# Optimization experiments

Measured on AMD Instinct MI355X. Metric: run time of the kernel, lower is better.

## Reference

```python
import jax, jax.numpy as jnp
import numpy as np

Q_HEADS, KV_HEADS, DIMS, IN_DIMS = 16, 4, 1024, 1024
HEAD_D = DIMS // Q_HEADS            # 64
GROUPS = Q_HEADS // KV_HEADS        # 4
ROPE_BASE = 10000.0


def nd_rope(x, coords):
    """N-D rotary embedding.
    x: [..., s, d]; coords: broadcastable [..., s, a] (float).
    Head dim d is split into a contiguous chunks of d//a; within each chunk
    consecutive pairs (2i, 2i+1) are rotated by angle coord_axis * base^(-2i/(d//a)).
    """
    a = coords.shape[-1]
    d = x.shape[-1]
    dpa = d // a                                  # dims per coordinate axis (even)
    inv_freq = ROPE_BASE ** (-jnp.arange(dpa // 2, dtype=jnp.float32) * (2.0 / dpa))
    angles = coords[..., :, None] * inv_freq      # [..., s, a, dpa//2]
    angles = angles.reshape(angles.shape[:-2] + (d // 2,))
    cos, sin = jnp.cos(angles), jnp.sin(angles)
    xp = x.reshape(x.shape[:-1] + (d // 2, 2))
    x1, x2 = xp[..., 0], xp[..., 1]
    return jnp.stack([x1 * cos - x2 * sin, x1 * sin + x2 * cos], axis=-1).reshape(x.shape)


def setup_inputs() -> dict:
    key = jax.random.key(0)
    k1, k2, k3, k4, k5, k6, k7, k8 = jax.random.split(key, 8)
    B, SQ, SKV, A = 4, 2048, 2048, 2
    q = jax.random.normal(k1, (B, SQ, IN_DIMS), dtype=jnp.float32)
    kv = jax.random.normal(k2, (B, SKV, IN_DIMS), dtype=jnp.float32)
    q_coords = jax.random.randint(k3, (B, SQ, A), 0, 2048, dtype=jnp.int32)
    kv_coords = jax.random.randint(k4, (B, SKV, A), 0, 2048, dtype=jnp.int32)
    s_in = 1.0 / np.sqrt(IN_DIMS)
    Wq = jax.random.normal(k5, (IN_DIMS, Q_HEADS, HEAD_D), dtype=jnp.float32) * s_in
    Wk = jax.random.normal(k6, (IN_DIMS, KV_HEADS, HEAD_D), dtype=jnp.float32) * s_in
    Wv = jax.random.normal(k7, (IN_DIMS, KV_HEADS, HEAD_D), dtype=jnp.float32) * s_in
    Wo = jax.random.normal(k8, (KV_HEADS * HEAD_D, IN_DIMS), dtype=jnp.float32) * (1.0 / np.sqrt(KV_HEADS * HEAD_D))
    return {"q": q, "q_coords": q_coords, "kv": kv, "kv_coords": kv_coords,
            "Wq": Wq, "Wk": Wk, "Wv": Wv, "Wo": Wo}


def reference(q, q_coords, kv, kv_coords, Wq, Wk, Wv, Wo):
    B, SQ = q.shape[0], q.shape[1]
    qp = jnp.einsum('bsi,ihd->bshd', q, Wq)   # [b, sq, q_heads, hd]
    kp = jnp.einsum('bsi,ihd->bshd', kv, Wk)  # [b, skv, kv_heads, hd]
    vp = jnp.einsum('bsi,ihd->bshd', kv, Wv)
    # '... s (h g) d -> ... g h s d' with h=KV_HEADS outer, g=GROUPS inner
    qp = qp.reshape(B, SQ, KV_HEADS, GROUPS, HEAD_D).transpose(0, 3, 2, 1, 4)  # [b,g,h,sq,hd]
    kp = kp.transpose(0, 2, 1, 3)  # [b,h,skv,hd]
    vp = vp.transpose(0, 2, 1, 3)
    qc = q_coords.astype(jnp.float32)[:, None, None]  # [b,1,1,sq,a] -> broadcast over g,h
    kc = kv_coords.astype(jnp.float32)[:, None]       # [b,1,skv,a] -> broadcast over h
    qr = nd_rope(qp, qc)
    kr = nd_rope(kp, kc)
    # NOTE: einops pattern omits g in output -> group axis is SUMMED (faithful to source)
    scores = jnp.einsum('bghsd,bhad->bhsa', qr, kr) / (HEAD_D ** 0.5)
    attn = jax.nn.softmax(scores, axis=-1)
    out = jnp.einsum('bhsa,bhad->bhsd', attn, vp)
    out = out.transpose(0, 2, 1, 3).reshape(B, SQ, KV_HEADS * HEAD_D)
    return out @ Wo
```

## Files before the change

### kernel.cpp

```cpp
#include <hip/hip_runtime.h>

#define BATCH 4
#define SEQQ  2048
#define SEQKV 2048
#define NH    4
#define HD    64
#define IND   1024
#define QSCL 0.18033688011112042f

typedef __attribute__((ext_vector_type(8))) short short8;
typedef __attribute__((ext_vector_type(4))) short s4v;
typedef __attribute__((ext_vector_type(4))) float floatx4;

#if defined(__HIP_DEVICE_COMPILE__) && __has_builtin(__builtin_amdgcn_exp2f)
  #define EXP2(x) __builtin_amdgcn_exp2f(x)
#else
  #define EXP2(x) exp2f(x)
#endif

#if defined(__HIP_DEVICE_COMPILE__)
  #if __has_builtin(__builtin_amdgcn_mfma_f32_16x16x16bf16_1k)
    #define MFMA16(a, b, c) __builtin_amdgcn_mfma_f32_16x16x16bf16_1k(a, b, c, 0, 0, 0)
  #elif __has_builtin(__builtin_amdgcn_mfma_f32_16x16x16_bf16)
    #define MFMA16(a, b, c) __builtin_amdgcn_mfma_f32_16x16x16_bf16(a, b, c, 0, 0, 0)
  #else
    #error "no 16x16x16 bf16 MFMA builtin on gfx950 device pass"
  #endif
#else
  #define MFMA16(a, b, c) (c)
#endif
#define MFMA32(a, b, c) __builtin_amdgcn_mfma_f32_16x16x32_bf16(a, b, c, 0, 0, 0)

__device__ __forceinline__ short f2b(float f) {
    unsigned u; __builtin_memcpy(&u, &f, 4);
    u = (u + 0x7fffu + ((u >> 16) & 1u)) >> 16;
    return (short)u;
}
__device__ __forceinline__ short8 cvt8(const float* p) {
    float4 a = *(const float4*)p;
    float4 b = *(const float4*)(p + 4);
    short8 r;
    r[0] = f2b(a.x); r[1] = f2b(a.y); r[2] = f2b(a.z); r[3] = f2b(a.w);
    r[4] = f2b(b.x); r[5] = f2b(b.y); r[6] = f2b(b.z); r[7] = f2b(b.w);
    return r;
}

__global__ __launch_bounds__(256) void prep_all(
    const float* __restrict__ Wq, const float* __restrict__ Wk,
    const float* __restrict__ Wv, const float* __restrict__ Wo,
    const float* __restrict__ q, const float* __restrict__ kv,
    short* __restrict__ Wq_t, short* __restrict__ Wkv_t, short* __restrict__ Wo_t,
    short* __restrict__ qb, short* __restrict__ kvb) {
    __shared__ short Ts[64][65];
    int blk = blockIdx.x;
    if (blk < 256) {
        int c4 = threadIdx.x & 63, r4 = threadIdx.x >> 6;
        if (blk < 64) {
            int h = blk & 3, ib = blk >> 2;
#pragma unroll 4
            for (int jj = 0; jj < 16; ++jj) {
                int il = r4 * 16 + jj;
                float s = 0.f;
#pragma unroll
                for (int g = 0; g < 4; ++g)
                    s += Wq[(ib * 64 + il) * 1024 + (h * 4 + g) * 64 + c4];
                Ts[il][c4] = f2b(s);
            }
            __syncthreads();
#pragma unroll 4
            for (int jj = 0; jj < 16; ++jj) {
                int dl = r4 * 16 + jj;
                Wq_t[(h * 64 + dl) * 1024 + ib * 64 + c4] = Ts[c4][dl];
            }
        } else if (blk < 192) {
            int t = blk - 64, ss = t >> 6; t &= 63;
            int ib = t >> 2, nb = t & 3;
            const float* W = ss ? Wv : Wk;
#pragma unroll 4
            for (int jj = 0; jj < 16; ++jj) {
                int il = r4 * 16 + jj;
                Ts[il][c4] = f2b(W[(ib * 64 + il) * 256 + nb * 64 + c4]);
            }
            __syncthreads();
#pragma unroll 4
            for (int jj = 0; jj < 16; ++jj) {
                int dl = r4 * 16 + jj;
                Wkv_t[(ss * 256 + nb * 64 + dl) * 1024 + ib * 64 + c4] = Ts[c4][dl];
            }
        } else {
            int t = blk - 192, kb = t >> 4, nb = t & 15;
#pragma unroll 4
            for (int jj = 0; jj < 16; ++jj) {
                int il = r4 * 16 + jj;
                Ts[il][c4] = f2b(Wo[(kb * 64 + il) * 1024 + nb * 64 + c4]);
            }
            __syncthreads();
#pragma unroll 4
            for (int jj = 0; jj < 16; ++jj) {
                int dl = r4 * 16 + jj;
                Wo_t[(nb * 64 + dl) * 256 + kb * 64 + c4] = Ts[c4][dl];
            }
        }
    } else if (blk < 2304) {
        long e = ((long)(blk - 256) * 256 + threadIdx.x) * 16;
        *(short8*)(qb + e)     = cvt8(q + e);
        *(short8*)(qb + e + 8) = cvt8(q + e + 8);
    } else {
        long e = ((long)(blk - 2304) * 256 + threadIdx.x) * 16;
        *(short8*)(kvb + e)     = cvt8(kv + e);
        *(short8*)(kvb + e + 8) = cvt8(kv + e + 8);
    }
}

template <int MODE>
__device__ __forceinline__ void gemm64(
    const short* __restrict__ A, const short* __restrict__ Wt,
    int m0, int n0, short* As, short* Bs,
    const int* __restrict__ coords, short* __restrict__ ropeDst,
    short* __restrict__ vDst) {
    const int t = threadIdx.x;
    const int w = t >> 6, lane = t & 63, ln = lane & 15, quad = lane >> 4;
    const int srow8 = lane >> 3;
    const int schk = (lane & 7) ^ (srow8 & 7);
    const int ln7 = ln & 7;
    floatx4 acc[2][4];
#pragma unroll
    for (int mt = 0; mt < 2; ++mt)
#pragma unroll
        for (int nt = 0; nt < 4; ++nt) acc[mt][nt] = floatx4{0.f, 0.f, 0.f, 0.f};

    auto stage = [&](int ks, int sel) {
#pragma unroll
        for (int i = 0; i < 4; ++i)
            __builtin_amdgcn_global_load_lds(
                (const void*)(A + (long)(m0 + w * 32 + i * 8 + srow8) * 1024 + ks + schk * 8),
                (void*)(As + sel * 8192 + (w * 32 + i * 8) * 64), 16, 0, 0);
#pragma unroll
        for (int i = 0; i < 2; ++i)
            __builtin_amdgcn_global_load_lds(
                (const void*)(Wt + (long)(n0 + w * 16 + i * 8 + srow8) * 1024 + ks + schk * 8),
                (void*)(Bs + sel * 4096 + (w * 16 + i * 8) * 64), 16, 0, 0);
    };

    stage(0, 0);
    __syncthreads();
    int cur = 0;
    for (int tt = 0; tt < 16; ++tt) {
        if (tt < 15) stage((tt + 1) * 64, cur ^ 1);
        const short* Ac = As + cur * 8192;
        const short* Bc = Bs + cur * 4096;
        short8 af[2][2], bf[4][2];
#pragma unroll
        for (int mt = 0; mt < 2; ++mt)
#pragma unroll
            for (int kc = 0; kc < 2; ++kc)
                af[mt][kc] = *(const short8*)(Ac + (w * 32 + mt * 16 + ln) * 64
                                              + ((kc * 4 + quad) ^ ln7) * 8);
#pragma unroll
        for (int nt = 0; nt < 4; ++nt)
#pragma unroll
            for (int kc = 0; kc < 2; ++kc)
                bf[nt][kc] = *(const short8*)(Bc + (nt * 16 + ln) * 64
                                              + ((kc * 4 + quad) ^ ln7) * 8);
#pragma unroll
        for (int kc = 0; kc < 2; ++kc)
#pragma unroll
            for (int mt = 0; mt < 2; ++mt)
#pragma unroll
                for (int nt = 0; nt < 4; ++nt)
                    acc[mt][nt] = MFMA32(af[mt][kc], bf[nt][kc], acc[mt][nt]);
        __syncthreads();
        cur ^= 1;
    }

    if (MODE == 1 || n0 < 256) {
        const int h = (n0 >> 6) & 3;
        const float scl = (MODE == 1) ? QSCL : 1.0f;
        const float L = -0.5756462732485114f;
        const float fA = __expf((float)(ln >> 1) * L);
        const float fB = __expf((float)(8 + (ln >> 1)) * L);
        const float sgn = (ln & 1) ? 1.0f : -1.0f;
#pragma unroll
        for (int mt = 0; mt < 2; ++mt) {
            int row0 = m0 + w * 32 + mt * 16 + quad * 4;
#pragma unroll
            for (int r = 0; r < 4; ++r) {
                int row = row0 + r;
                float c0 = (float)coords[row * 2];
                float c1 = (float)coords[row * 2 + 1];
                float snv[4], csv[4];
                __sincosf(c0 * fA, &snv[0], &csv[0]);
                __sincosf(c0 * fB, &snv[1], &csv[1]);
                __sincosf(c1 * fA, &snv[2], &csv[2]);
                __sincosf(c1 * fB, &snv[3], &csv[3]);
                long rbase = ((long)((row >> 11) * 4 + h) * 2048 + (row & 2047)) * 64;
#pragma unroll
                for (int nt = 0; nt < 4; ++nt) {
                    float v = acc[mt][nt][r];
                    float p = __shfl_xor(v, 1, 64);
                    float o = v * (csv[nt] * scl) + p * (snv[nt] * (scl * sgn));
                    ropeDst[rbase + nt * 16 + ln] = f2b(o);
                }
            }
        }
    } else {
        const int h = ((n0 - 256) >> 6) & 3;
#pragma unroll
        for (int mt = 0; mt < 2; ++mt) {
            int row0 = m0 + w * 32 + mt * 16 + quad * 4;
            int b = row0 >> 11, s0 = row0 & 2047;
#pragma unroll
            for (int nt = 0; nt < 4; ++nt) {
                s4v ov;
#pragma unroll
                for (int r = 0; r < 4; ++r) ov[r] = f2b(acc[mt][nt][r]);
                *(s4v*)(vDst + (long)((b * 4 + h) * 64 + nt * 16 + ln) * 2048 + s0) = ov;
            }
        }
    }
}

__global__ __launch_bounds__(256, 3) void proj_gemm(
    const short* __restrict__ qb, const short* __restrict__ kvb,
    const short* __restrict__ Wq_t, const short* __restrict__ Wkv_t,
    const int* __restrict__ qc, const int* __restrict__ kvc,
    short* __restrict__ Qr, short* __restrict__ Kr, short* __restrict__ Vt) {
    __shared__ __align__(16) short As[2 * 8192];
    __shared__ __align__(16) short Bs[2 * 4096];
    int id = (blockIdx.x & 7) * 96 + (blockIdx.x >> 3);
    if (id < 256)
        gemm64<1>(qb, Wq_t, (id >> 2) * 128, (id & 3) * 64, As, Bs, qc, Qr, nullptr);
    else {
        int t2 = id - 256;
        gemm64<2>(kvb, Wkv_t, (t2 >> 3) * 128, (t2 & 7) * 64, As, Bs, kvc, Kr, Vt);
    }
}

__global__ __launch_bounds__(256, 2) void final_gemm(
    const short* __restrict__ Ob, const short* __restrict__ Wo_t, float* __restrict__ out) {
    __shared__ __align__(16) short As[2 * 8192];
    __shared__ __align__(16) short Bs[2 * 8192];
    const int m0 = blockIdx.x * 128, n0 = blockIdx.y * 128;
    const int tid = threadIdx.x;
    const int w = tid >> 6, lane = tid & 63, ln = lane & 15, quad = lane >> 4;
    const int wm = w >> 1, wn = w & 1;
    const int srow8 = lane >> 3;
    const int schk = (lane & 7) ^ (srow8 & 7);
    const int ln7 = ln & 7;
    floatx4 acc[4][4];
#pragma unroll
    for (int mt = 0; mt < 4; ++mt)
#pragma unroll
        for (int nt = 0; nt < 4; ++nt) acc[mt][nt] = floatx4{0.f, 0.f, 0.f, 0.f};

    auto stage = [&](int ks, int sel) {
#pragma unroll
        for (int i = 0; i < 4; ++i) {
            __builtin_amdgcn_global_load_lds(
                (const void*)(Ob + (long)(m0 + w * 32 + i * 8 + srow8) * 256 + ks + schk * 8),
                (void*)(As + sel * 8192 + (w * 32 + i * 8) * 64), 16, 0, 0);
            __builtin_amdgcn_global_load_lds(
                (const void*)(Wo_t + (long)(n0 + w * 32 + i * 8 + srow8) * 256 + ks + schk * 8),
                (void*)(Bs + sel * 8192 + (w * 32 + i * 8) * 64), 16, 0, 0);
        }
    };
    stage(0, 0);
    __syncthreads();
    int cur = 0;
    for (int tt = 0; tt < 4; ++tt) {
        if (tt < 3) stage((tt + 1) * 64, cur ^ 1);
        const short* Ac = As + cur * 8192;
        const short* Bc = Bs + cur * 8192;
        short8 af[4][2], bf[4][2];
#pragma unroll
        for (int mt = 0; mt < 4; ++mt)
#pragma unroll
            for (int kc = 0; kc < 2; ++kc)
                af[mt][kc] = *(const short8*)(Ac + (wm * 64 + mt * 16 + ln) * 64
                                              + ((kc * 4 + quad) ^ ln7) * 8);
#pragma unroll
        for (int nt = 0; nt < 4; ++nt)
#pragma unroll
            for (int kc = 0; kc < 2; ++kc)
                bf[nt][kc] = *(const short8*)(Bc + (wn * 64 + nt * 16 + ln) * 64
                                              + ((kc * 4 + quad) ^ ln7) * 8);
#pragma unroll
        for (int kc = 0; kc < 2; ++kc)
#pragma unroll
            for (int mt = 0; mt < 4; ++mt)
#pragma unroll
                for (int nt = 0; nt < 4; ++nt)
                    acc[mt][nt] = MFMA32(af[mt][kc], bf[nt][kc], acc[mt][nt]);
        __syncthreads();
        cur ^= 1;
    }
#pragma unroll
    for (int mt = 0; mt < 4; ++mt) {
        int row0 = m0 + wm * 64 + mt * 16 + quad * 4;
#pragma unroll
        for (int nt = 0; nt < 4; ++nt) {
            int col = n0 + wn * 64 + nt * 16 + ln;
#pragma unroll
            for (int r = 0; r < 4; ++r)
                out[(long)(row0 + r) * 1024 + col] = acc[mt][nt][r];
        }
    }
}

__global__ __launch_bounds__(512, 4) void attn_kernel(
    const short* __restrict__ Qr, const short* __restrict__ Kr,
    const short* __restrict__ Vt, short* __restrict__ Ob) {
    __shared__ __align__(16) short Kls[2][2][64 * 64];
    __shared__ __align__(16) short Vls[2][2][64 * 64];
    const int blk = blockIdx.x;
    const int x = blk & 7, y = blk >> 3;
    const int bh = x * 2 + (y >> 5), qg = y & 31;
    const int w = threadIdx.x >> 6, lane = threadIdx.x & 63;
    const int qw = w & 3, half = w >> 2;
    const int ln = lane & 15, quad = lane >> 4;
    const int q0 = qg * 64 + qw * 16;
    const short* Qb = Qr + (long)bh * SEQKV * HD;
    const short* Kb = Kr + (long)bh * SEQKV * HD + (long)half * 1024 * HD;
    const short* Vb = Vt + (long)bh * HD * SEQKV + half * 1024;

    const int srow = lane >> 3;
    const int schk = (lane & 7) ^ (srow & 7);
    const long kstage0 = (long)(qw * 16 + srow) * HD + schk * 8;
    const long vstage0 = (long)(qw * 16 + srow) * SEQKV + schk * 8;

    short8 qf[2];
#pragma unroll
    for (int ck = 0; ck < 2; ++ck)
        qf[ck] = *(const short8*)(Qb + (long)(q0 + ln) * HD + ck * 32 + quad * 8);

    s4v ones;
#pragma unroll
    for (int j = 0; j < 4; ++j) ones[j] = (short)0x3F80;

    floatx4 o[4], ol;
    ol = floatx4{0.f, 0.f, 0.f, 0.f};
#pragma unroll
    for (int nt = 0; nt < 4; ++nt) o[nt] = floatx4{0.f, 0.f, 0.f, 0.f};

    const int ln7 = ln & 7;
    int koff[2];
#pragma unroll
    for (int ck = 0; ck < 2; ++ck) koff[ck] = ln * 64 + ((ck * 4 + quad) ^ ln7) * 8;
    int voff[4];
#pragma unroll
    for (int t = 0; t < 4; ++t) voff[t] = ln * 64 + ((t * 2 + (quad >> 1)) ^ ln7) * 8 + (quad & 1) * 4;

#define STAGE(kt, sel)                                                                \
    do {                                                                              \
        _Pragma("unroll")                                                             \
        for (int i = 0; i < 2; ++i) {                                                 \
            __builtin_amdgcn_global_load_lds(                                         \
                (const void*)(Kb + (long)(kt) * HD + kstage0 + (long)i * 8 * HD),     \
                (void*)(&Kls[half][sel][(qw * 16 + i * 8) * 64]), 16, 0, 0);          \
            __builtin_amdgcn_global_load_lds(                                         \
                (const void*)(Vb + (kt) + vstage0 + (long)i * 8 * SEQKV),             \
                (void*)(&Vls[half][sel][(qw * 16 + i * 8) * 64]), 16, 0, 0);          \
        }                                                                             \
    } while (0)

    STAGE(0, 0);
    __syncthreads();
    int cur = 0;
    for (int tt = 0; tt < 16; ++tt) {
        if (tt < 15) STAGE((tt + 1) * 64, cur ^ 1);
        const short* Kc = &Kls[half][cur][0];
        const short* Vc = &Vls[half][cur][0];
#pragma unroll
        for (int t = 0; t < 4; ++t) {
            short8 a0 = *(const short8*)(Kc + t * 1024 + koff[0]);
            short8 a1 = *(const short8*)(Kc + t * 1024 + koff[1]);
            floatx4 st = {0.f, 0.f, 0.f, 0.f};
            __builtin_amdgcn_s_setprio(1);
            st = MFMA32(a0, qf[0], st);
            st = MFMA32(a1, qf[1], st);
            __builtin_amdgcn_s_setprio(0);
            float e0 = EXP2(st[0]), e1 = EXP2(st[1]), e2 = EXP2(st[2]), e3 = EXP2(st[3]);
            unsigned p0, p1;
            asm("v_cvt_pk_bf16_f32 %0, %1, %2" : "=v"(p0) : "v"(e0), "v"(e1));
            asm("v_cvt_pk_bf16_f32 %0, %1, %2" : "=v"(p1) : "v"(e2), "v"(e3));
            s4v pt;
            { unsigned tmp[2] = {p0, p1}; __builtin_memcpy(&pt, tmp, 8); }
            __builtin_amdgcn_s_setprio(1);
#pragma unroll
            for (int nt = 0; nt < 4; ++nt) {
                s4v vf = *(const s4v*)(Vc + nt * 1024 + voff[t]);
                o[nt] = MFMA16(vf, pt, o[nt]);
            }
            ol = MFMA16(ones, pt, ol);
            __builtin_amdgcn_s_setprio(0);
        }
        __syncthreads();
        cur ^= 1;
    }
#undef STAGE
    float* cb = (float*)&Kls[0][0][0];
    const int slot = (qw * 64 + lane) * 20;
    if (half == 1) {
#pragma unroll
        for (int nt = 0; nt < 4; ++nt)
            *(floatx4*)(cb + slot + nt * 4) = o[nt];
        cb[slot + 16] = ol[0];
    }
    __syncthreads();
    if (half == 0) {
        const int b = bh >> 2, h = bh & 3;
        const float li = 1.0f / (ol[0] + cb[slot + 16]);
        const long base = ((long)(b * 2048 + q0 + ln)) * 256 + h * 64;
#pragma unroll
        for (int nt = 0; nt < 4; ++nt) {
            floatx4 o2 = *(const floatx4*)(cb + slot + nt * 4);
            s4v ov;
#pragma unroll
            for (int r = 0; r < 4; ++r) ov[r] = f2b((o[nt][r] + o2[r]) * li);
            *(s4v*)(Ob + base + nt * 16 + quad * 4) = ov;
        }
    }
}

extern "C" void kernel_launch(void* const* d_in, const int* in_sizes, int n_in,
                              void* d_out, int out_size, void* d_ws, size_t ws_size,
                              hipStream_t stream) {
    const float* q   = (const float*)d_in[0];
    const int*   qc  = (const int*)d_in[1];
    const float* kv  = (const float*)d_in[2];
    const int*   kvc = (const int*)d_in[3];
    const float* Wq  = (const float*)d_in[4];
    const float* Wk  = (const float*)d_in[5];
    const float* Wv  = (const float*)d_in[6];
    const float* Wo  = (const float*)d_in[7];
    float* out = (float*)d_out;

    char* ws = (char*)d_ws;
    const size_t MB = 1024 * 1024;
    short* Wq_t  = (short*)(ws);
    short* Wkv_t = (short*)(ws + MB / 2);
    short* Wo_t  = (short*)(ws + 3 * MB / 2);
    short* qb    = (short*)(ws + 2 * MB);
    short* kvb   = (short*)(ws + 18 * MB);
    short* Qr    = (short*)(ws + 34 * MB);
    short* Kr    = (short*)(ws + 38 * MB);
    short* Vt    = (short*)(ws + 42 * MB);
    short* Ob    = (short*)(ws + 46 * MB);

    hipLaunchKernelGGL(prep_all, dim3(4352), dim3(256), 0, stream,
                       Wq, Wk, Wv, Wo, q, kv, Wq_t, Wkv_t, Wo_t, qb, kvb);
    hipLaunchKernelGGL(proj_gemm, dim3(768), dim3(256), 0, stream,
                       qb, kvb, Wq_t, Wkv_t, qc, kvc, Qr, Kr, Vt);
    hipLaunchKernelGGL(attn_kernel, dim3(512), dim3(512), 0, stream,
                       Qr, Kr, Vt, Ob);
    hipLaunchKernelGGL(final_gemm, dim3(64, 8), dim3(256), 0, stream, Ob, Wo_t, out);
}
```

Measured before the change: 178.6 us.

## Process two query subtiles per wave in attention, halving block threads

The attention kernel now uses 4 waves per block instead of 8. Each wave handles 32 query rows as two 16-row subtiles, so every K and V fragment read from LDS feeds twice as many MFMAs. Each wave also stages twice as many K/V rows. This cuts LDS read traffic per FLOP and the instruction overhead around it, at the cost of more registers per wave and less parallelism per block. Launch bounds change to (256,2), which may lower occupancy and the ability to hide latency.

```diff
diff --git a/kernel.cpp b/kernel.cpp
--- a/kernel.cpp
+++ b/kernel.cpp
@@ -307,7 +307,7 @@
     }
 }
 
-__global__ __launch_bounds__(512, 4) void attn_kernel(
+__global__ __launch_bounds__(256, 2) void attn_kernel(
     const short* __restrict__ Qr, const short* __restrict__ Kr,
     const short* __restrict__ Vt, short* __restrict__ Ob) {
     __shared__ __align__(16) short Kls[2][2][64 * 64];
@@ -316,31 +316,36 @@
     const int x = blk & 7, y = blk >> 3;
     const int bh = x * 2 + (y >> 5), qg = y & 31;
     const int w = threadIdx.x >> 6, lane = threadIdx.x & 63;
-    const int qw = w & 3, half = w >> 2;
+    const int u = w & 1, half = w >> 1;
     const int ln = lane & 15, quad = lane >> 4;
-    const int q0 = qg * 64 + qw * 16;
+    const int q0 = qg * 64 + u * 32;
     const short* Qb = Qr + (long)bh * SEQKV * HD;
     const short* Kb = Kr + (long)bh * SEQKV * HD + (long)half * 1024 * HD;
     const short* Vb = Vt + (long)bh * HD * SEQKV + half * 1024;
 
     const int srow = lane >> 3;
     const int schk = (lane & 7) ^ (srow & 7);
-    const long kstage0 = (long)(qw * 16 + srow) * HD + schk * 8;
-    const long vstage0 = (long)(qw * 16 + srow) * SEQKV + schk * 8;
-
-    short8 qf[2];
-#pragma unroll
-    for (int ck = 0; ck < 2; ++ck)
-        qf[ck] = *(const short8*)(Qb + (long)(q0 + ln) * HD + ck * 32 + quad * 8);
+    const long kstage0 = (long)(u * 32 + srow) * HD + schk * 8;
+    const long vstage0 = (long)(u * 32 + srow) * SEQKV + schk * 8;
+
+    short8 qf[2][2];
+#pragma unroll
+    for (int qs = 0; qs < 2; ++qs)
+#pragma unroll
+        for (int ck = 0; ck < 2; ++ck)
+            qf[qs][ck] = *(const short8*)(Qb + (long)(q0 + qs * 16 + ln) * HD + ck * 32 + quad * 8);
 
     s4v ones;
 #pragma unroll
     for (int j = 0; j < 4; ++j) ones[j] = (short)0x3F80;
 
-    floatx4 o[4], ol;
-    ol = floatx4{0.f, 0.f, 0.f, 0.f};
-#pragma unroll
-    for (int nt = 0; nt < 4; ++nt) o[nt] = floatx4{0.f, 0.f, 0.f, 0.f};
+    floatx4 o[2][4], ol[2];
+#pragma unroll
+    for (int qs = 0; qs < 2; ++qs) {
+        ol[qs] = floatx4{0.f, 0.f, 0.f, 0.f};
+#pragma unroll
+        for (int nt = 0; nt < 4; ++nt) o[qs][nt] = floatx4{0.f, 0.f, 0.f, 0.f};
+    }
 
     const int ln7 = ln & 7;
     int koff[2];
@@ -353,13 +358,13 @@
 #define STAGE(kt, sel)                                                                \
     do {                                                                              \
         _Pragma("unroll")                                                             \
-        for (int i = 0; i < 2; ++i) {                                                 \
+        for (int i = 0; i < 4; ++i) {                                                 \
             __builtin_amdgcn_global_load_lds(                                         \
                 (const void*)(Kb + (long)(kt) * HD + kstage0 + (long)i * 8 * HD),     \
-                (void*)(&Kls[half][sel][(qw * 16 + i * 8) * 64]), 16, 0, 0);          \
+                (void*)(&Kls[half][sel][(u * 32 + i * 8) * 64]), 16, 0, 0);           \
             __builtin_amdgcn_global_load_lds(                                         \
                 (const void*)(Vb + (kt) + vstage0 + (long)i * 8 * SEQKV),             \
-                (void*)(&Vls[half][sel][(qw * 16 + i * 8) * 64]), 16, 0, 0);          \
+                (void*)(&Vls[half][sel][(u * 32 + i * 8) * 64]), 16, 0, 0);           \
         }                                                                             \
     } while (0)
 
@@ -374,24 +379,32 @@
         for (int t = 0; t < 4; ++t) {
             short8 a0 = *(const short8*)(Kc + t * 1024 + koff[0]);
             short8 a1 = *(const short8*)(Kc + t * 1024 + koff[1]);
-            floatx4 st = {0.f, 0.f, 0.f, 0.f};
+            floatx4 st0 = {0.f, 0.f, 0.f, 0.f}, st1 = {0.f, 0.f, 0.f, 0.f};
             __builtin_amdgcn_s_setprio(1);
-            st = MFMA32(a0, qf[0], st);
-            st = MFMA32(a1, qf[1], st);
+            st0 = MFMA32(a0, qf[0][0], st0);
+            st1 = MFMA32(a0, qf[1][0], st1);
+            st0 = MFMA32(a1, qf[0][1], st0);
+            st1 = MFMA32(a1, qf[1][1], st1);
             __builtin_amdgcn_s_setprio(0);
-            float e0 = EXP2(st[0]), e1 = EXP2(st[1]), e2 = EXP2(st[2]), e3 = EXP2(st[3]);
-            unsigned p0, p1;
-            asm("v_cvt_pk_bf16_f32 %0, %1, %2" : "=v"(p0) : "v"(e0), "v"(e1));
-            asm("v_cvt_pk_bf16_f32 %0, %1, %2" : "=v"(p1) : "v"(e2), "v"(e3));
-            s4v pt;
-            { unsigned tmp[2] = {p0, p1}; __builtin_memcpy(&pt, tmp, 8); }
+            float e0 = EXP2(st0[0]), e1 = EXP2(st0[1]), e2 = EXP2(st0[2]), e3 = EXP2(st0[3]);
+            float g0 = EXP2(st1[0]), g1 = EXP2(st1[1]), g2 = EXP2(st1[2]), g3 = EXP2(st1[3]);
+            unsigned a0p, a1p, b0p, b1p;
+            asm("v_cvt_pk_bf16_f32 %0, %1, %2" : "=v"(a0p) : "v"(e0), "v"(e1));
+            asm("v_cvt_pk_bf16_f32 %0, %1, %2" : "=v"(a1p) : "v"(e2), "v"(e3));
+            asm("v_cvt_pk_bf16_f32 %0, %1, %2" : "=v"(b0p) : "v"(g0), "v"(g1));
+            asm("v_cvt_pk_bf16_f32 %0, %1, %2" : "=v"(b1p) : "v"(g2), "v"(g3));
+            s4v pt0, pt1;
+            { unsigned tmp[2] = {a0p, a1p}; __builtin_memcpy(&pt0, tmp, 8); }
+            { unsigned tmp[2] = {b0p, b1p}; __builtin_memcpy(&pt1, tmp, 8); }
             __builtin_amdgcn_s_setprio(1);
 #pragma unroll
             for (int nt = 0; nt < 4; ++nt) {
                 s4v vf = *(const s4v*)(Vc + nt * 1024 + voff[t]);
-                o[nt] = MFMA16(vf, pt, o[nt]);
-            }
-            ol = MFMA16(ones, pt, ol);
+                o[0][nt] = MFMA16(vf, pt0, o[0][nt]);
+                o[1][nt] = MFMA16(vf, pt1, o[1][nt]);
+            }
+            ol[0] = MFMA16(ones, pt0, ol[0]);
+            ol[1] = MFMA16(ones, pt1, ol[1]);
             __builtin_amdgcn_s_setprio(0);
         }
         __syncthreads();
@@ -399,25 +412,31 @@
     }
 #undef STAGE
     float* cb = (float*)&Kls[0][0][0];
-    const int slot = (qw * 64 + lane) * 20;
+    const int slot = (u * 64 + lane) * 36;
     if (half == 1) {
 #pragma unroll
-        for (int nt = 0; nt < 4; ++nt)
-            *(floatx4*)(cb + slot + nt * 4) = o[nt];
-        cb[slot + 16] = ol[0];
+        for (int qs = 0; qs < 2; ++qs)
+#pragma unroll
+            for (int nt = 0; nt < 4; ++nt)
+                *(floatx4*)(cb + slot + (qs * 4 + nt) * 4) = o[qs][nt];
+        cb[slot + 32] = ol[0][0];
+        cb[slot + 33] = ol[1][0];
     }
     __syncthreads();
     if (half == 0) {
         const int b = bh >> 2, h = bh & 3;
-        const float li = 1.0f / (ol[0] + cb[slot + 16]);
-        const long base = ((long)(b * 2048 + q0 + ln)) * 256 + h * 64;
-#pragma unroll
-        for (int nt = 0; nt < 4; ++nt) {
-            floatx4 o2 = *(const floatx4*)(cb + slot + nt * 4);
-            s4v ov;
-#pragma unroll
-            for (int r = 0; r < 4; ++r) ov[r] = f2b((o[nt][r] + o2[r]) * li);
-            *(s4v*)(Ob + base + nt * 16 + quad * 4) = ov;
+#pragma unroll
+        for (int qs = 0; qs < 2; ++qs) {
+            const float li = 1.0f / (ol[qs][0] + cb[slot + 32 + qs]);
+            const long base = ((long)(b * 2048 + q0 + qs * 16 + ln)) * 256 + h * 64;
+#pragma unroll
+            for (int nt = 0; nt < 4; ++nt) {
+                floatx4 o2 = *(const floatx4*)(cb + slot + (qs * 4 + nt) * 4);
+                s4v ov;
+#pragma unroll
+                for (int r = 0; r < 4; ++r) ov[r] = f2b((o[qs][nt][r] + o2[r]) * li);
+                *(s4v*)(Ob + base + nt * 16 + quad * 4) = ov;
+            }
         }
     }
 }
@@ -451,7 +470,7 @@
                        Wq, Wk, Wv, Wo, q, kv, Wq_t, Wkv_t, Wo_t, qb, kvb);
     hipLaunchKernelGGL(proj_gemm, dim3(768), dim3(256), 0, stream,
                        qb, kvb, Wq_t, Wkv_t, qc, kvc, Qr, Kr, Vt);
-    hipLaunchKernelGGL(attn_kernel, dim3(512), dim3(512), 0, stream,
+    hipLaunchKernelGGL(attn_kernel, dim3(512), dim3(256), 0, stream,
                        Qr, Kr, Vt, Ob);
     hipLaunchKernelGGL(final_gemm, dim3(64, 8), dim3(256), 0, stream, Ob, Wo_t, out);
 }
```

Measured after the change: 180.0 us. No clear change (+0.8%).
